# Performance work log

Measured on AMD Instinct MI355X. Metric: run time of the kernel, lower is better.

Reference implementation:

```python
import jax, jax.numpy as jnp
import numpy as np

V = 1_000_000   # variables
F = 4_200_000   # functions (clauses), ratio ~4.2
K = 3           # literals per clause
E = K * F       # edges
T = 5           # fixed number of peel iterations (peel update is idempotent once converged)


def setup_inputs() -> dict:
    key = jax.random.key(0)
    k1, k2 = jax.random.split(key, 2)
    vidx = jax.random.randint(k1, (E,), 0, V, dtype=jnp.int32)
    fidx = jnp.repeat(jnp.arange(F, dtype=jnp.int32), K)  # each clause touches K variables
    graph_map = jnp.stack([vidx, fidx])  # [2, E]
    edge_feature = (2 * jax.random.randint(k2, (E,), 0, 2) - 1).astype(jnp.float32)  # +/-1 literal signs
    active_variables = jnp.ones((V, 1), jnp.float32)
    active_functions = jnp.ones((F, 1), jnp.float32)
    return dict(graph_map=graph_map, edge_feature=edge_feature,
                active_variables=active_variables, active_functions=active_functions)


def reference(graph_map, edge_feature, active_variables, active_functions):
    """Peeling propagation over the bipartite variable-function graph.

    Equivalent to the torch sparse-mm formulation:
      vf_map @ x        == segment_sum(x[fidx], vidx, V)
      signed_vf_map @ x == segment_sum(edge_feature * x[fidx], vidx, V)
      vf_map^T @ y      == segment_sum(y[vidx], fidx, F)
    """
    nV = active_variables.shape[0]
    nF = active_functions.shape[0]
    vidx = graph_map[0]
    fidx = graph_map[1]
    ef = edge_feature[:, None]  # [E,1]

    def seg_v(x_f):        # vf_map @ x_f : [F,1] -> [V,1]
        return jax.ops.segment_sum(x_f[fidx], vidx, num_segments=nV)

    def seg_v_signed(x_f):  # signed_vf_map @ x_f
        return jax.ops.segment_sum(ef * x_f[fidx], vidx, num_segments=nV)

    def seg_f(x_v):        # vf_map^T @ x_v : [V,1] -> [F,1]
        return jax.ops.segment_sum(x_v[vidx], fidx, num_segments=nF)

    variable_degree = seg_v(active_functions)
    signed_variable_degree = seg_v_signed(active_functions)

    def step(carry, _):
        av, af, deg, sdeg = carry
        # variables whose active clause occurrences all share one sign
        single_v = (deg == jnp.abs(sdeg)).astype(deg.dtype) * av
        # active clauses touched by those variables become satisfied
        single_f = (seg_f(single_v) > 0).astype(af.dtype) * af
        deg = deg - seg_v(single_f) * av
        sdeg = sdeg - seg_v_signed(single_f) * av
        av = av * (1.0 - single_v)
        af = af * (1.0 - single_f)
        return (av, af, deg, sdeg), None

    (av, af, deg, sdeg), _ = jax.lax.scan(
        step, (active_variables, active_functions, variable_degree, signed_variable_degree),
        None, length=T)
    return deg  # residual variable degrees after peeling [V,1]
```

## Files before the change

### kernel.cpp

```cpp
#include <hip/hip_runtime.h>


static constexpr int Vn = 1000000;
static constexpr int Fn = 4200000;
static constexpr int Tn = 5;

static constexpr int SBLK = 2048;
static constexpr int FPB  = 2052;
static constexpr int BIN_BITS = 10;
static constexpr int BIN_SIZE = 1 << BIN_BITS;
static constexpr int NB  = (Vn + BIN_SIZE - 1) >> BIN_BITS;
static constexpr int NBP = 1024;
static constexpr int CH_BITS = 11;
static constexpr int CH_SIZE = 1 << CH_BITS;
static constexpr int NCH = (Vn + CH_SIZE - 1) >> CH_BITS;
static constexpr int RCAP = 3 * FPB;
static constexpr int RSTRIDE = (RCAP + 63) & ~63;
static constexpr int OROW = 1024;
static constexpr int AVW = NCH * (CH_SIZE / 64);

__global__ __launch_bounds__(256) void k_pack_sort(
    const int* __restrict__ vidx, const float* __restrict__ ef,
    const float* __restrict__ afunc,
    unsigned long long* __restrict__ gpack,
    unsigned short* __restrict__ offs,
    unsigned short* __restrict__ sorted)
{
    __shared__ unsigned int cur[NBP];
    __shared__ unsigned int wsum[4];
    __shared__ unsigned int s_total;
    __shared__ __align__(16) unsigned short st[RSTRIDE];

    const int k = blockIdx.x;
    const int f0 = k * FPB;
    int n = Fn - f0; if (n < 0) n = 0; if (n > FPB) n = FPB;
    const int n4 = n >> 2;
    const int t = threadIdx.x;

    for (int i = t; i < NBP; i += 256) cur[i] = 0u;
    __syncthreads();

    const int j0 = t, j1 = t + 256, j2 = t + 512;
    const bool has0 = j0 < n4, has1 = j1 < n4, has2 = j2 < n4;
    unsigned long long q0a=0,q0b=0,q0c=0,q0d=0, q1a=0,q1b=0,q1c=0,q1d=0, q2a=0,q2b=0,q2c=0,q2d=0;

#define PROC(J, QA, QB, QC, QD) do {                                               \
    const int fb = f0 + 4 * (J), e = 3 * fb;                                       \
    int4 va = *(const int4*)(vidx + e);                                            \
    int4 vb = *(const int4*)(vidx + e + 4);                                        \
    int4 vc = *(const int4*)(vidx + e + 8);                                        \
    float4 ea = *(const float4*)(ef + e);                                          \
    float4 eb = *(const float4*)(ef + e + 4);                                      \
    float4 ec = *(const float4*)(ef + e + 8);                                      \
    float4 a4 = *(const float4*)(afunc + fb);                                      \
    int   vv[12] = {va.x,va.y,va.z,va.w,vb.x,vb.y,vb.z,vb.w,vc.x,vc.y,vc.z,vc.w};  \
    float ss[12] = {ea.x,ea.y,ea.z,ea.w,eb.x,eb.y,eb.z,eb.w,ec.x,ec.y,ec.z,ec.w};  \
    float aa[4]  = {a4.x,a4.y,a4.z,a4.w};                                          \
    unsigned long long gq[4];                                                      \
    _Pragma("unroll")                                                              \
    for (int q = 0; q < 4; ++q) {                                                  \
        int v0 = vv[3*q], v1 = vv[3*q+1], v2 = vv[3*q+2];                          \
        unsigned int s0 = ss[3*q]   > 0.0f ? 1u : 0u;                              \
        unsigned int s1 = ss[3*q+1] > 0.0f ? 1u : 0u;                              \
        unsigned int s2 = ss[3*q+2] > 0.0f ? 1u : 0u;                              \
        unsigned int act = aa[q] != 0.0f ? 1u : 0u;                                \
        gq[q] = (unsigned long long)(unsigned int)v0                               \
              | ((unsigned long long)(unsigned int)v1 << 20)                       \
              | ((unsigned long long)(unsigned int)v2 << 40)                       \
              | ((unsigned long long)s0 << 60)                                     \
              | ((unsigned long long)s1 << 61)                                     \
              | ((unsigned long long)s2 << 62)                                     \
              | ((unsigned long long)act << 63);                                   \
        if (act) {                                                                 \
            atomicAdd(&cur[v0 >> BIN_BITS], 1u);                                   \
            atomicAdd(&cur[v1 >> BIN_BITS], 1u);                                   \
            atomicAdd(&cur[v2 >> BIN_BITS], 1u);                                   \
        }                                                                          \
    }                                                                              \
    *(ulonglong2*)(gpack + fb)     = make_ulonglong2(gq[0], gq[1]);                \
    *(ulonglong2*)(gpack + fb + 2) = make_ulonglong2(gq[2], gq[3]);                \
    QA = gq[0]; QB = gq[1]; QC = gq[2]; QD = gq[3];                                \
} while (0)

    if (has0) PROC(j0, q0a, q0b, q0c, q0d);
    if (has1) PROC(j1, q1a, q1b, q1c, q1d);
    if (has2) PROC(j2, q2a, q2b, q2c, q2d);
#undef PROC
    __syncthreads();

    {
        const int lane = t & 63, wid = t >> 6;
        unsigned int a0 = cur[4 * t], a1 = cur[4 * t + 1];
        unsigned int a2 = cur[4 * t + 2], a3 = cur[4 * t + 3];
        unsigned int tsum = a0 + a1 + a2 + a3;
        unsigned int x = tsum;
        #pragma unroll
        for (int off = 1; off < 64; off <<= 1) {
            unsigned int y = (unsigned int)__shfl_up((int)x, off);
            if (lane >= off) x += y;
        }
        if (lane == 63) wsum[wid] = x;
        __syncthreads();
        unsigned int wbase = 0;
        for (int w = 0; w < wid; ++w) wbase += wsum[w];
        unsigned int e0x = wbase + x - tsum;
        unsigned int e1x = e0x + a0, e2x = e1x + a1, e3x = e2x + a2;
        cur[4 * t] = e0x; cur[4 * t + 1] = e1x; cur[4 * t + 2] = e2x; cur[4 * t + 3] = e3x;
        if (t == 255) s_total = e3x + a3;
        unsigned short* row = offs + (size_t)k * OROW;
        if (4 * t     <= NB) row[4 * t]     = (unsigned short)e0x;
        if (4 * t + 1 <= NB) row[4 * t + 1] = (unsigned short)e1x;
        if (4 * t + 2 <= NB) row[4 * t + 2] = (unsigned short)e2x;
        if (4 * t + 3 <= NB) row[4 * t + 3] = (unsigned short)e3x;
    }
    __syncthreads();

#define SCAT1(G) do {                                                              \
    unsigned long long g = (G);                                                    \
    if ((long long)g < 0) {                                                        \
        unsigned int v0 = (unsigned int)(g & 0xFFFFFu);                            \
        unsigned int v1 = (unsigned int)((g >> 20) & 0xFFFFFu);                    \
        unsigned int v2 = (unsigned int)((g >> 40) & 0xFFFFFu);                    \
        unsigned int sl0 = atomicAdd(&cur[v0 >> BIN_BITS], 1u);                    \
        st[sl0] = (unsigned short)((v0 & (CH_SIZE-1)) | ((unsigned int)((g >> 60) & 1u) << CH_BITS)); \
        unsigned int sl1 = atomicAdd(&cur[v1 >> BIN_BITS], 1u);                    \
        st[sl1] = (unsigned short)((v1 & (CH_SIZE-1)) | ((unsigned int)((g >> 61) & 1u) << CH_BITS)); \
        unsigned int sl2 = atomicAdd(&cur[v2 >> BIN_BITS], 1u);                    \
        st[sl2] = (unsigned short)((v2 & (CH_SIZE-1)) | ((unsigned int)((g >> 62) & 1u) << CH_BITS)); \
    }                                                                              \
} while (0)
    if (has0) { SCAT1(q0a); SCAT1(q0b); SCAT1(q0c); SCAT1(q0d); }
    if (has1) { SCAT1(q1a); SCAT1(q1b); SCAT1(q1c); SCAT1(q1d); }
    if (has2) { SCAT1(q2a); SCAT1(q2b); SCAT1(q2c); SCAT1(q2d); }
#undef SCAT1
    __syncthreads();

    {
        const int tot = (int)s_total;
        const int nvec = (tot + 7) >> 3;
        int4* __restrict__ dst = (int4*)(sorted + (size_t)k * RSTRIDE);
        const int4* __restrict__ src = (const int4*)st;
        for (int i = t; i < nvec; i += 256) dst[i] = src[i];
    }
}

__device__ __forceinline__ unsigned short subdirty4(unsigned long long m) {
    unsigned int r = 0;
    #pragma unroll
    for (int j = 0; j < 16; ++j)
        r |= (((m >> (4 * j)) & 0xFull) ? 1u : 0u) << j;
    return (unsigned short)r;
}

__global__ __launch_bounds__(1024) void k_accum(
    const unsigned short* __restrict__ offs,
    const unsigned short* __restrict__ sorted,
    const float* __restrict__ avars,
    unsigned int* __restrict__ packed,
    unsigned long long* __restrict__ avm,
    unsigned long long* __restrict__ svm,
    unsigned short* __restrict__ sgrp4,
    unsigned int* __restrict__ tmp,
    unsigned char* __restrict__ tgrp)
{
    __shared__ unsigned int acc[CH_SIZE];
    __shared__ unsigned short row0[SBLK];
    __shared__ unsigned short row1[SBLK];
    const int c = blockIdx.x;
    const int r0 = 2 * c;
    const int r1 = (2 * c + 2 < NB) ? (2 * c + 2) : NB;
    for (int i = threadIdx.x; i < CH_SIZE; i += 1024) acc[i] = 0u;
    for (int i = threadIdx.x; i < SBLK; i += 1024) {
        row0[i] = offs[(size_t)i * OROW + r0];
        row1[i] = offs[(size_t)i * OROW + r1];
    }
    __syncthreads();
    for (int k = threadIdx.x; k < SBLK; k += 1024) {
        const int s0 = row0[k], s1 = row1[k];
        const unsigned short* seg = sorted + (size_t)k * RSTRIDE;
        int e = s0;
        for (; e < s1 && (e & 3); ++e) {
            unsigned int p = seg[e];
            atomicAdd(&acc[p & (CH_SIZE - 1)], 0x10000u | (p >> CH_BITS));
        }
        for (; e + 4 <= s1; e += 4) {
            unsigned long long q = *(const unsigned long long*)(seg + e);
            #pragma unroll
            for (int j = 0; j < 4; ++j) {
                unsigned int p = (unsigned int)((q >> (16 * j)) & 0xFFFFu);
                atomicAdd(&acc[p & (CH_SIZE - 1)], 0x10000u | (p >> CH_BITS));
            }
        }
        for (; e < s1; ++e) {
            unsigned int p = seg[e];
            atomicAdd(&acc[p & (CH_SIZE - 1)], 0x10000u | (p >> CH_BITS));
        }
    }
    __syncthreads();
    const int vbase = c << CH_BITS;
    for (int i = threadIdx.x; i < CH_SIZE; i += 1024) {
        int v = vbase + i;
        bool valid = v < Vn;
        unsigned int p = valid ? acc[i] : 0u;
        bool av = valid && (avars[v] != 0.0f);
        unsigned int cnt = p >> 16, pos = p & 0xFFFFu;
        bool sv = av && (pos == 0u || pos == cnt);
        unsigned long long avb = __ballot(av);
        unsigned long long svb = __ballot(sv);
        if (valid) { packed[v] = p; tmp[v] = 0u; }
        if ((threadIdx.x & 63) == 0) {
            avm[v >> 6] = avb;
            svm[v >> 6] = svb;
            sgrp4[v >> 6] = subdirty4(svb);
            tgrp[v >> 6] = 0;
        }
    }
}

__device__ __forceinline__ void fire_one(unsigned long long g, int f,
                                         unsigned long long* __restrict__ gpack,
                                         const unsigned int* __restrict__ svm32,
                                         const unsigned short* __restrict__ s4,
                                         unsigned int* __restrict__ tmp,
                                         unsigned char* __restrict__ tgrp)
{
    if ((long long)g >= 0) return;
    unsigned int v0 = (unsigned int)(g & 0xFFFFFu);
    unsigned int v1 = (unsigned int)((g >> 20) & 0xFFFFFu);
    unsigned int v2 = (unsigned int)((g >> 40) & 0xFFFFFu);
    unsigned int h0 = (unsigned int)(s4[v0 >> 6] >> ((v0 >> 2) & 15u)) & 1u;
    unsigned int h1 = (unsigned int)(s4[v1 >> 6] >> ((v1 >> 2) & 15u)) & 1u;
    unsigned int h2 = (unsigned int)(s4[v2 >> 6] >> ((v2 >> 2) & 15u)) & 1u;
    if (!(h0 | h1 | h2)) return;
    unsigned int hit = ((svm32[v0 >> 5] >> (v0 & 31u)) |
                        (svm32[v1 >> 5] >> (v1 & 31u)) |
                        (svm32[v2 >> 5] >> (v2 & 31u))) & 1u;
    if (!hit) return;
    gpack[f] = g & ~(1ull << 63);
    atomicAdd(&tmp[v0], 0x10000u | (unsigned int)((g >> 60) & 1u));
    atomicAdd(&tmp[v1], 0x10000u | (unsigned int)((g >> 61) & 1u));
    atomicAdd(&tmp[v2], 0x10000u | (unsigned int)((g >> 62) & 1u));
    tgrp[v0 >> 6] = 1; tgrp[v1 >> 6] = 1; tgrp[v2 >> 6] = 1;
}

static constexpr int FBLOCKS = 1024;

__global__ __launch_bounds__(256) void k_funcs(unsigned long long* __restrict__ gpack,
                        const unsigned int* __restrict__ svm32,
                        const unsigned short* __restrict__ sgrp4,
                        unsigned int* __restrict__ tmp,
                        unsigned char* __restrict__ tgrp)
{
    __shared__ __align__(16) unsigned short s4[AVW];
    for (int i = threadIdx.x; i < AVW / 8; i += 256)
        ((int4*)s4)[i] = ((const int4*)sgrp4)[i];
    __syncthreads();
    const int step = FBLOCKS * 256 * 8;
    for (int f = (blockIdx.x * 256 + threadIdx.x) * 8; f < Fn; f += step) {
        ulonglong2 ga = *(const ulonglong2*)(gpack + f);
        ulonglong2 gb = *(const ulonglong2*)(gpack + f + 2);
        ulonglong2 gc = *(const ulonglong2*)(gpack + f + 4);
        ulonglong2 gd = *(const ulonglong2*)(gpack + f + 6);
        fire_one(ga.x, f,     gpack, svm32, s4, tmp, tgrp);
        fire_one(ga.y, f + 1, gpack, svm32, s4, tmp, tgrp);
        fire_one(gb.x, f + 2, gpack, svm32, s4, tmp, tgrp);
        fire_one(gb.y, f + 3, gpack, svm32, s4, tmp, tgrp);
        fire_one(gc.x, f + 4, gpack, svm32, s4, tmp, tgrp);
        fire_one(gc.y, f + 5, gpack, svm32, s4, tmp, tgrp);
        fire_one(gd.x, f + 6, gpack, svm32, s4, tmp, tgrp);
        fire_one(gd.y, f + 7, gpack, svm32, s4, tmp, tgrp);
    }
}

__global__ void k_update(unsigned int* __restrict__ packed,
                         unsigned int* __restrict__ tmp,
                         unsigned long long* __restrict__ avm,
                         unsigned long long* __restrict__ svm,
                         unsigned short* __restrict__ sgrp4,
                         unsigned char* __restrict__ tgrp,
                         float* __restrict__ deg, int write_deg)
{
    const int v = blockIdx.x * blockDim.x + threadIdx.x;
    const int lane = threadIdx.x & 63;
    const bool valid = v < Vn;
    unsigned long long avw = 0ull, svw = 0ull;
    unsigned char tg = 0;
    if (valid) {
        avw = avm[v >> 6]; svw = svm[v >> 6];
        tg = tgrp[v >> 6];
    }
    if (!write_deg && !tg && svw == 0ull) return;
    const bool av_old = valid && ((avw >> lane) & 1ull);
    const bool sv     = valid && ((svw >> lane) & 1ull);
    const bool av_new = av_old && !sv;
    unsigned int p = 0u;
    if (valid) {
        p = packed[v];
        if (tg) {
            unsigned int tp = tmp[v];
            if (tp != 0u) {
                if (av_old) { p -= tp; packed[v] = p; }
                tmp[v] = 0u;
            }
        }
    }
    const unsigned int c = p >> 16, pos = p & 0xFFFFu;
    const bool nsv = av_new && (pos == 0u || pos == c);
    unsigned long long nsvb = __ballot(nsv);
    if (lane == 0 && valid) {
        svm[v >> 6] = nsvb;
        avm[v >> 6] = avw & ~svw;
        sgrp4[v >> 6] = subdirty4(nsvb);
        if (tg) tgrp[v >> 6] = 0;
    }
    if (write_deg && valid) deg[v] = (float)c;
}

extern "C" void kernel_launch(void* const* d_in, const int* in_sizes, int n_in,
                              void* d_out, int out_size, void* d_ws, size_t ws_size,
                              hipStream_t stream) {
    const int*   graph_map        = (const int*)d_in[0];
    const float* edge_feature     = (const float*)d_in[1];
    const float* active_variables = (const float*)d_in[2];
    const float* active_functions = (const float*)d_in[3];
    const int* vidx = graph_map;

    float* deg = (float*)d_out;
    char* ws = (char*)d_ws;
    size_t off = 0;
    auto alloc = [&](size_t bytes) -> void* {
        void* p = ws + off; off += (bytes + 255) & ~(size_t)255; return p;
    };
    unsigned long long* gpack = (unsigned long long*)alloc(8ull * Fn);
    unsigned int* packed      = (unsigned int*)alloc(4ull * Vn);
    unsigned long long* avm   = (unsigned long long*)alloc(8ull * AVW);
    unsigned long long* svm   = (unsigned long long*)alloc(8ull * AVW);
    unsigned short* sgrp4     = (unsigned short*)alloc(2ull * AVW);
    unsigned char* tgrp       = (unsigned char*)alloc(AVW);
    unsigned short* offs      = (unsigned short*)alloc(2ull * SBLK * OROW);
    unsigned short* sorted    = (unsigned short*)alloc(2ull * SBLK * RSTRIDE);
    unsigned int* tmp         = (unsigned int*)alloc(4ull * Vn);

    const int BS = 256;
    const int gV = (Vn + BS - 1) / BS;

    k_pack_sort<<<SBLK, 256, 0, stream>>>(vidx, edge_feature, active_functions,
                                          gpack, offs, sorted);
    k_accum<<<NCH, 1024, 0, stream>>>(offs, sorted, active_variables, packed,
                                      avm, svm, sgrp4, tmp, tgrp);
    for (int t = 0; t < Tn; ++t) {
        k_funcs<<<FBLOCKS, BS, 0, stream>>>(gpack, (const unsigned int*)svm, sgrp4, tmp, tgrp);
        k_update<<<gV, BS, 0, stream>>>(packed, tmp, avm, svm, sgrp4, tgrp, deg, (t == Tn - 1) ? 1 : 0);
    }
}
```

Before: 334.0 us.

## Apply clause peel decrements directly to packed degrees and widen accum chunks

Fired clauses now atomically subtract from the packed degree word of each still-active variable, gated by the active-variable bitmask. This removes the separate tmp accumulator, its zeroing in k_accum, and the read-modify-write merge in k_update. The accum chunk size is doubled (CH_BITS 11 to 12), so each block covers four bins and half as many blocks are launched. Atomics now hit the live packed array and add an extra avm lookup per literal, and the larger chunk changes block count and shared memory use.

```diff
diff --git a/kernel.cpp b/kernel.cpp
--- a/kernel.cpp
+++ b/kernel.cpp
@@ -11,7 +11,7 @@
 static constexpr int BIN_SIZE = 1 << BIN_BITS;
 static constexpr int NB  = (Vn + BIN_SIZE - 1) >> BIN_BITS;
 static constexpr int NBP = 1024;
-static constexpr int CH_BITS = 11;
+static constexpr int CH_BITS = 12;
 static constexpr int CH_SIZE = 1 << CH_BITS;
 static constexpr int NCH = (Vn + CH_SIZE - 1) >> CH_BITS;
 static constexpr int RCAP = 3 * FPB;
@@ -160,15 +160,14 @@
     unsigned long long* __restrict__ avm,
     unsigned long long* __restrict__ svm,
     unsigned short* __restrict__ sgrp4,
-    unsigned int* __restrict__ tmp,
     unsigned char* __restrict__ tgrp)
 {
     __shared__ unsigned int acc[CH_SIZE];
     __shared__ unsigned short row0[SBLK];
     __shared__ unsigned short row1[SBLK];
     const int c = blockIdx.x;
-    const int r0 = 2 * c;
-    const int r1 = (2 * c + 2 < NB) ? (2 * c + 2) : NB;
+    const int r0 = 4 * c;
+    const int r1 = (4 * c + 4 < NB) ? (4 * c + 4) : NB;
     for (int i = threadIdx.x; i < CH_SIZE; i += 1024) acc[i] = 0u;
     for (int i = threadIdx.x; i < SBLK; i += 1024) {
         row0[i] = offs[(size_t)i * OROW + r0];
@@ -207,7 +206,7 @@
         bool sv = av && (pos == 0u || pos == cnt);
         unsigned long long avb = __ballot(av);
         unsigned long long svb = __ballot(sv);
-        if (valid) { packed[v] = p; tmp[v] = 0u; }
+        if (valid) packed[v] = p;
         if ((threadIdx.x & 63) == 0) {
             avm[v >> 6] = avb;
             svm[v >> 6] = svb;
@@ -220,8 +219,9 @@
 __device__ __forceinline__ void fire_one(unsigned long long g, int f,
                                          unsigned long long* __restrict__ gpack,
                                          const unsigned int* __restrict__ svm32,
+                                         const unsigned int* __restrict__ avm32,
                                          const unsigned short* __restrict__ s4,
-                                         unsigned int* __restrict__ tmp,
+                                         unsigned int* __restrict__ packed,
                                          unsigned char* __restrict__ tgrp)
 {
     if ((long long)g >= 0) return;
@@ -237,9 +237,12 @@
                         (svm32[v2 >> 5] >> (v2 & 31u))) & 1u;
     if (!hit) return;
     gpack[f] = g & ~(1ull << 63);
-    atomicAdd(&tmp[v0], 0x10000u | (unsigned int)((g >> 60) & 1u));
-    atomicAdd(&tmp[v1], 0x10000u | (unsigned int)((g >> 61) & 1u));
-    atomicAdd(&tmp[v2], 0x10000u | (unsigned int)((g >> 62) & 1u));
+    if ((avm32[v0 >> 5] >> (v0 & 31u)) & 1u)
+        atomicSub(&packed[v0], 0x10000u | (unsigned int)((g >> 60) & 1u));
+    if ((avm32[v1 >> 5] >> (v1 & 31u)) & 1u)
+        atomicSub(&packed[v1], 0x10000u | (unsigned int)((g >> 61) & 1u));
+    if ((avm32[v2 >> 5] >> (v2 & 31u)) & 1u)
+        atomicSub(&packed[v2], 0x10000u | (unsigned int)((g >> 62) & 1u));
     tgrp[v0 >> 6] = 1; tgrp[v1 >> 6] = 1; tgrp[v2 >> 6] = 1;
 }
 
@@ -247,8 +250,9 @@
 
 __global__ __launch_bounds__(256) void k_funcs(unsigned long long* __restrict__ gpack,
                         const unsigned int* __restrict__ svm32,
+                        const unsigned int* __restrict__ avm32,
                         const unsigned short* __restrict__ sgrp4,
-                        unsigned int* __restrict__ tmp,
+                        unsigned int* __restrict__ packed,
                         unsigned char* __restrict__ tgrp)
 {
     __shared__ __align__(16) unsigned short s4[AVW];
@@ -261,19 +265,18 @@
         ulonglong2 gb = *(const ulonglong2*)(gpack + f + 2);
         ulonglong2 gc = *(const ulonglong2*)(gpack + f + 4);
         ulonglong2 gd = *(const ulonglong2*)(gpack + f + 6);
-        fire_one(ga.x, f,     gpack, svm32, s4, tmp, tgrp);
-        fire_one(ga.y, f + 1, gpack, svm32, s4, tmp, tgrp);
-        fire_one(gb.x, f + 2, gpack, svm32, s4, tmp, tgrp);
-        fire_one(gb.y, f + 3, gpack, svm32, s4, tmp, tgrp);
-        fire_one(gc.x, f + 4, gpack, svm32, s4, tmp, tgrp);
-        fire_one(gc.y, f + 5, gpack, svm32, s4, tmp, tgrp);
-        fire_one(gd.x, f + 6, gpack, svm32, s4, tmp, tgrp);
-        fire_one(gd.y, f + 7, gpack, svm32, s4, tmp, tgrp);
-    }
-}
-
-__global__ void k_update(unsigned int* __restrict__ packed,
-                         unsigned int* __restrict__ tmp,
+        fire_one(ga.x, f,     gpack, svm32, avm32, s4, packed, tgrp);
+        fire_one(ga.y, f + 1, gpack, svm32, avm32, s4, packed, tgrp);
+        fire_one(gb.x, f + 2, gpack, svm32, avm32, s4, packed, tgrp);
+        fire_one(gb.y, f + 3, gpack, svm32, avm32, s4, packed, tgrp);
+        fire_one(gc.x, f + 4, gpack, svm32, avm32, s4, packed, tgrp);
+        fire_one(gc.y, f + 5, gpack, svm32, avm32, s4, packed, tgrp);
+        fire_one(gd.x, f + 6, gpack, svm32, avm32, s4, packed, tgrp);
+        fire_one(gd.y, f + 7, gpack, svm32, avm32, s4, packed, tgrp);
+    }
+}
+
+__global__ void k_update(const unsigned int* __restrict__ packed,
                          unsigned long long* __restrict__ avm,
                          unsigned long long* __restrict__ svm,
                          unsigned short* __restrict__ sgrp4,
@@ -293,17 +296,7 @@
     const bool av_old = valid && ((avw >> lane) & 1ull);
     const bool sv     = valid && ((svw >> lane) & 1ull);
     const bool av_new = av_old && !sv;
-    unsigned int p = 0u;
-    if (valid) {
-        p = packed[v];
-        if (tg) {
-            unsigned int tp = tmp[v];
-            if (tp != 0u) {
-                if (av_old) { p -= tp; packed[v] = p; }
-                tmp[v] = 0u;
-            }
-        }
-    }
+    unsigned int p = valid ? packed[v] : 0u;
     const unsigned int c = p >> 16, pos = p & 0xFFFFu;
     const bool nsv = av_new && (pos == 0u || pos == c);
     unsigned long long nsvb = __ballot(nsv);
@@ -339,7 +332,6 @@
     unsigned char* tgrp       = (unsigned char*)alloc(AVW);
     unsigned short* offs      = (unsigned short*)alloc(2ull * SBLK * OROW);
     unsigned short* sorted    = (unsigned short*)alloc(2ull * SBLK * RSTRIDE);
-    unsigned int* tmp         = (unsigned int*)alloc(4ull * Vn);
 
     const int BS = 256;
     const int gV = (Vn + BS - 1) / BS;
@@ -347,9 +339,10 @@
     k_pack_sort<<<SBLK, 256, 0, stream>>>(vidx, edge_feature, active_functions,
                                           gpack, offs, sorted);
     k_accum<<<NCH, 1024, 0, stream>>>(offs, sorted, active_variables, packed,
-                                      avm, svm, sgrp4, tmp, tgrp);
+                                      avm, svm, sgrp4, tgrp);
     for (int t = 0; t < Tn; ++t) {
-        k_funcs<<<FBLOCKS, BS, 0, stream>>>(gpack, (const unsigned int*)svm, sgrp4, tmp, tgrp);
-        k_update<<<gV, BS, 0, stream>>>(packed, tmp, avm, svm, sgrp4, tgrp, deg, (t == Tn - 1) ? 1 : 0);
-    }
-}
+        k_funcs<<<FBLOCKS, BS, 0, stream>>>(gpack, (const unsigned int*)svm,
+                                            (const unsigned int*)avm, sgrp4, packed, tgrp);
+        k_update<<<gV, BS, 0, stream>>>(packed, avm, svm, sgrp4, tgrp, deg, (t == Tn - 1) ? 1 : 0);
+    }
+}
```

New measurement: 314.0 us. 6.0% less time.
